# Performance work log

Measured on AMD Instinct MI355X. Metric: run time of the kernel, lower is better.

The kernel has to match this reference:

```python
import jax, jax.numpy as jnp
import numpy as np

B, S, D, H, HD, LY, DY = 2, 2048, 2048, 16, 128, 512, 2048
EPS_QK = 1e-5   # torch LayerNorm default for q_norm/k_norm
EPS_KY = 1e-6   # ky_norm eps


def _layernorm(x, w, b, eps):
    mu = jnp.mean(x, axis=-1, keepdims=True)
    var = jnp.mean(jnp.square(x - mu), axis=-1, keepdims=True)
    return (x - mu) * jax.lax.rsqrt(var + eps) * w + b


def _rope(t, freqs_cis):
    # t: [b, s, h, d]; freqs_cis: [s, d//2, 2] = (cos, sin)
    b, s, h, d = t.shape
    t2 = t.reshape(b, s, h, d // 2, 2)
    cos = freqs_cis[None, :, None, :, 0]
    sin = freqs_cis[None, :, None, :, 1]
    r0 = t2[..., 0] * cos - t2[..., 1] * sin
    r1 = t2[..., 0] * sin + t2[..., 1] * cos
    return jnp.stack([r0, r1], axis=-1).reshape(b, s, h, d)


def _attn(q, k, v, kv_mask, scale):
    # q: [b,s,h,d], k/v: [b,t,h,d], kv_mask: [b,t] bool
    scores = jnp.einsum('bshd,bthd->bhst', q, k) * scale
    neg = jnp.finfo(scores.dtype).min
    scores = jnp.where(kv_mask[:, None, None, :], scores, neg)
    p = jax.nn.softmax(scores, axis=-1)
    return jnp.einsum('bhst,bthd->bshd', p, v)


def setup_inputs() -> dict:
    key = jax.random.key(0)
    ks = jax.random.split(key, 20)
    x = jax.random.normal(ks[0], (B, S, D), jnp.float32)
    y = jax.random.normal(ks[1], (B, LY, DY), jnp.float32)
    x_mask = jnp.ones((B, S), jnp.bool_)
    y_mask = jnp.ones((B, LY), jnp.bool_)
    # RoPE table, theta=10000
    pos = jnp.arange(S, dtype=jnp.float32)
    inv = 1.0 / (10000.0 ** (jnp.arange(0, HD, 2, dtype=jnp.float32) / HD))
    ang = pos[:, None] * inv[None, :]                      # [S, HD//2]
    freqs_cis = jnp.stack([jnp.cos(ang), jnp.sin(ang)], -1)  # [S, HD//2, 2]
    sd = 0.02
    wq = sd * jax.random.normal(ks[2], (D, H * HD), jnp.float32)
    wk = sd * jax.random.normal(ks[3], (D, H * HD), jnp.float32)
    wv = sd * jax.random.normal(ks[4], (D, H * HD), jnp.float32)
    wo = sd * jax.random.normal(ks[5], (H * HD, D), jnp.float32)
    wky = sd * jax.random.normal(ks[6], (DY, H * HD), jnp.float32)
    wvy = sd * jax.random.normal(ks[7], (DY, H * HD), jnp.float32)
    gate = 0.1 * jax.random.normal(ks[8], (H,), jnp.float32)  # nn.Parameter (zeros init; randomized for nontrivial test)
    qn_w = 1.0 + 0.01 * jax.random.normal(ks[9], (H * HD,), jnp.float32)
    qn_b = 0.01 * jax.random.normal(ks[10], (H * HD,), jnp.float32)
    kn_w = 1.0 + 0.01 * jax.random.normal(ks[11], (H * HD,), jnp.float32)
    kn_b = 0.01 * jax.random.normal(ks[12], (H * HD,), jnp.float32)
    kyn_w = 1.0 + 0.01 * jax.random.normal(ks[13], (H * HD,), jnp.float32)
    kyn_b = 0.01 * jax.random.normal(ks[14], (H * HD,), jnp.float32)
    return dict(x=x, x_mask=x_mask, freqs_cis=freqs_cis, y=y, y_mask=y_mask,
                wq=wq, wk=wk, wv=wv, wo=wo, wky=wky, wvy=wvy, gate=gate,
                qn_w=qn_w, qn_b=qn_b, kn_w=kn_w, kn_b=kn_b, kyn_w=kyn_w, kyn_b=kyn_b)


def reference(x, x_mask, freqs_cis, y, y_mask, wq, wk, wv, wo, wky, wvy, gate,
              qn_w, qn_b, kn_w, kn_b, kyn_w, kyn_b):
    batch, seq_len, _ = x.shape
    xq = x @ wq
    xk = x @ wk
    xv = x @ wv
    # qk_norm with qk_bias=True: LayerNorm over full n_heads*head_dim channels
    xq = _layernorm(xq, qn_w, qn_b, EPS_QK)
    xk = _layernorm(xk, kn_w, kn_b, EPS_QK)
    xq = xq.reshape(batch, seq_len, H, HD)
    xk = xk.reshape(batch, seq_len, H, HD)
    xv = xv.reshape(batch, seq_len, H, HD)
    # n_kv_heads == n_heads: no repeat_interleave needed
    xq = _rope(xq, freqs_cis)
    xk = _rope(xk, freqs_cis)
    scale = 1.0 / jnp.sqrt(jnp.float32(HD))  # softmax_scale=None -> 1/sqrt(head_dim)
    output = _attn(xq, xk, xv, x_mask, scale)            # [b,s,h,d]
    # cross-attention branch (y_dim > 0); no RoPE on yk
    yk = _layernorm(y @ wky, kyn_w, kyn_b, EPS_KY).reshape(batch, -1, H, HD)
    yv = (y @ wvy).reshape(batch, -1, H, HD)
    output_y = _attn(xq, yk, yv, y_mask, scale)
    output_y = output_y * jnp.tanh(gate)[None, None, :, None]
    output = output + output_y
    out = output.reshape(batch, seq_len, H * HD) @ wo
    return out
```

## Files before the change

### kernel.cpp

```cpp
#include <hip/hip_runtime.h>

typedef unsigned short u16;
typedef __attribute__((ext_vector_type(8))) short short8;
typedef __attribute__((ext_vector_type(4))) unsigned short ushort4v;
typedef __attribute__((ext_vector_type(8))) unsigned short ushort8v;
typedef __attribute__((ext_vector_type(4))) float f32x4;

#define MFMA_16x16x32(a, b, c) __builtin_amdgcn_mfma_f32_16x16x32_bf16(a, b, c, 0, 0, 0)

#define GLOAD16(g, l)                                                              \
    __builtin_amdgcn_global_load_lds(                                              \
        (const __attribute__((address_space(1))) unsigned int*)(g),                \
        (__attribute__((address_space(3))) unsigned int*)(l), 16, 0, 0)

__device__ __forceinline__ u16 f2bf(float f) {
    unsigned int u = __float_as_uint(f);
    u += 0x7fffu + ((u >> 16) & 1u);
    return (u16)(u >> 16);
}

__global__ __launch_bounds__(256) void k_cast(const float* __restrict__ in, u16* __restrict__ out) {
    long i = ((long)blockIdx.x * 256 + threadIdx.x) * 8;
    f32x4 a = *(const f32x4*)(in + i);
    f32x4 b = *(const f32x4*)(in + i + 4);
    ushort8v o;
    o[0] = f2bf(a[0]); o[1] = f2bf(a[1]); o[2] = f2bf(a[2]); o[3] = f2bf(a[3]);
    o[4] = f2bf(b[0]); o[5] = f2bf(b[1]); o[6] = f2bf(b[2]); o[7] = f2bf(b[3]);
    *(ushort8v*)(out + i) = o;
}

__global__ __launch_bounds__(256) void k_tcast(const float* __restrict__ in, u16* __restrict__ out,
                                               int R, int C, long ibs, long obs) {
    __shared__ float tile[32][33];
    const int t = threadIdx.x;
    const int tx = t & 31, ty = t >> 5;
    const long r0 = (long)blockIdx.y * 32, c0 = (long)blockIdx.x * 32;
    const float* ip = in + (long)blockIdx.z * ibs;
    u16* op = out + (long)blockIdx.z * obs;
#pragma unroll
    for (int i = 0; i < 4; i++)
        tile[ty + 8 * i][tx] = ip[(r0 + ty + 8 * i) * C + c0 + tx];
    __syncthreads();
#pragma unroll
    for (int i = 0; i < 4; i++)
        op[(c0 + ty + 8 * i) * R + r0 + tx] = f2bf(tile[tx][ty + 8 * i]);
}

__device__ __forceinline__ void gemm_body(const u16* __restrict__ A, const u16* __restrict__ Bt,
                                          float* __restrict__ C, int N, int K) {
    __shared__ u16 As[128 * 32];
    __shared__ u16 Bs[128 * 32];
    const int t = threadIdx.x;
    const int lane = t & 63, wave = t >> 6;
    const long m0 = (long)blockIdx.y * 128, n0 = (long)blockIdx.x * 128;
    const int wm = (wave >> 1) * 64, wn = (wave & 1) * 64;
    const u16* Ag = A + (m0 + (t >> 2)) * (long)K + (t & 3) * 8;
    const u16* Bg = Bt + (n0 + (t >> 2)) * (long)K + (t & 3) * 8;
    u16* lA = As + wave * 512;
    u16* lB = Bs + wave * 512;
    const int fr = lane & 15, fg = (lane >> 4) * 8;
    const f32x4 z = {0.f, 0.f, 0.f, 0.f};
    f32x4 acc[4][4];
#pragma unroll
    for (int i = 0; i < 4; i++)
#pragma unroll
        for (int j = 0; j < 4; j++) acc[i][j] = z;
    for (int k0 = 0; k0 < K; k0 += 32) {
        __syncthreads();
        GLOAD16(Ag + k0, lA);
        GLOAD16(Ag + (long)64 * K + k0, lA + 2048);
        GLOAD16(Bg + k0, lB);
        GLOAD16(Bg + (long)64 * K + k0, lB + 2048);
        __syncthreads();
        short8 af[4], bf[4];
#pragma unroll
        for (int i = 0; i < 4; i++) {
            af[i] = *(const short8*)&As[(wm + i * 16 + fr) * 32 + fg];
            bf[i] = *(const short8*)&Bs[(wn + i * 16 + fr) * 32 + fg];
        }
#pragma unroll
        for (int i = 0; i < 4; i++)
#pragma unroll
            for (int j = 0; j < 4; j++)
                acc[i][j] = MFMA_16x16x32(af[i], bf[j], acc[i][j]);
    }
    const int cr = (lane >> 4) * 4, cc = lane & 15;
#pragma unroll
    for (int i = 0; i < 4; i++)
#pragma unroll
        for (int j = 0; j < 4; j++)
#pragma unroll
            for (int r = 0; r < 4; r++)
                C[(m0 + wm + i * 16 + cr + r) * N + (n0 + wn + j * 16 + cc)] = acc[i][j][r];
}

__global__ __launch_bounds__(256) void k_gemm(const u16* __restrict__ A, const u16* __restrict__ Bt,
                                              float* __restrict__ C, int N, int K) {
    gemm_body(A, Bt, C, N, K);
}

__global__ __launch_bounds__(256) void k_gemm2(const u16* __restrict__ A,
                                               const u16* __restrict__ Bt0, const u16* __restrict__ Bt1,
                                               float* __restrict__ C0, float* __restrict__ C1,
                                               int N, int K) {
    gemm_body(A, blockIdx.z ? Bt1 : Bt0, blockIdx.z ? C1 : C0, N, K);
}

__global__ __launch_bounds__(256) void k_ln(const float* __restrict__ in, const float* __restrict__ w,
                                            const float* __restrict__ bia, const float* __restrict__ freqs,
                                            u16* __restrict__ out, int Srows, float eps, int do_rope) {
    const int row = blockIdx.x;
    const int bi = row / Srows, s = row - bi * Srows;
    const int t = threadIdx.x;
    const long base = (long)row * 2048 + t * 8;
    f32x4 v0 = *(const f32x4*)(in + base);
    f32x4 v1 = *(const f32x4*)(in + base + 4);
    float sum = 0.f, sq = 0.f;
#pragma unroll
    for (int r = 0; r < 4; r++) {
        sum += v0[r] + v1[r];
        sq += v0[r] * v0[r] + v1[r] * v1[r];
    }
#pragma unroll
    for (int off = 32; off >= 1; off >>= 1) {
        sum += __shfl_xor(sum, off);
        sq += __shfl_xor(sq, off);
    }
    __shared__ float red[8];
    const int wv = t >> 6, lane = t & 63;
    if (lane == 0) { red[wv] = sum; red[4 + wv] = sq; }
    __syncthreads();
    sum = red[0] + red[1] + red[2] + red[3];
    sq  = red[4] + red[5] + red[6] + red[7];
    const float mu = sum * (1.f / 2048.f);
    const float rstd = rsqrtf(sq * (1.f / 2048.f) - mu * mu + eps);
    const int c0 = t * 8;
    f32x4 w0 = *(const f32x4*)(w + c0), w1 = *(const f32x4*)(w + c0 + 4);
    f32x4 b0 = *(const f32x4*)(bia + c0), b1 = *(const f32x4*)(bia + c0 + 4);
    float nv[8];
#pragma unroll
    for (int r = 0; r < 4; r++) {
        nv[r]     = (v0[r] - mu) * rstd * w0[r] + b0[r];
        nv[4 + r] = (v1[r] - mu) * rstd * w1[r] + b1[r];
    }
    if (do_rope) {
        const float* fp = freqs + ((long)s * 64 + ((c0 & 127) >> 1)) * 2;
        f32x4 f0 = *(const f32x4*)(fp), f1 = *(const f32x4*)(fp + 4);
        float t0, t1;
        t0 = nv[0]; t1 = nv[1]; nv[0] = t0 * f0[0] - t1 * f0[1]; nv[1] = t0 * f0[1] + t1 * f0[0];
        t0 = nv[2]; t1 = nv[3]; nv[2] = t0 * f0[2] - t1 * f0[3]; nv[3] = t0 * f0[3] + t1 * f0[2];
        t0 = nv[4]; t1 = nv[5]; nv[4] = t0 * f1[0] - t1 * f1[1]; nv[5] = t0 * f1[1] + t1 * f1[0];
        t0 = nv[6]; t1 = nv[7]; nv[6] = t0 * f1[2] - t1 * f1[3]; nv[7] = t0 * f1[3] + t1 * f1[2];
    }
    const int h = c0 >> 7;
    ushort8v o;
#pragma unroll
    for (int r = 0; r < 8; r++) o[r] = f2bf(nv[r]);
    *(ushort8v*)(out + (((long)bi * 16 + h) * Srows + s) * 128 + (c0 & 127)) = o;
}

__global__ __launch_bounds__(256, 4) void k_attn(const u16* __restrict__ Q, const u16* __restrict__ Kg,
                                                 const u16* __restrict__ Vt, const u16* __restrict__ Yk,
                                                 const u16* __restrict__ Yvt, const float* __restrict__ gate,
                                                 u16* __restrict__ Out) {
    __shared__ u16 Ks[2][32 * 128];
    __shared__ u16 Vs[2][128 * 32];
    __shared__ u16 Ps[4][16 * 40];
    const int t = threadIdx.x, lane = t & 63, wave = t >> 6;
    const int h = blockIdx.y, b = blockIdx.z;
    const int q0 = blockIdx.x * 64 + wave * 16;
    const long bh = (long)b * 16 + h;
    const int fr = lane & 15;
    const int g = lane >> 4;
    const int fg8 = g * 8;
    const float scale = 0.08838834764831845f;
    const f32x4 z = {0.f, 0.f, 0.f, 0.f};

    const int kr0 = (wave * 2 + 0) * 4 + (lane >> 4);
    const int kr1 = (wave * 2 + 1) * 4 + (lane >> 4);
    const int kc0 = ((lane & 15) ^ (kr0 & 7)) * 8;
    const int kc1 = ((lane & 15) ^ (kr1 & 7)) * 8;
    const int vr0 = (wave * 2 + 0) * 16 + (lane >> 2);
    const int vr1 = (wave * 2 + 1) * 16 + (lane >> 2);
    const int vc = (lane & 3) * 8;

    const u16* qp = Q + (bh * 2048 + q0 + fr) * 128;
    short8 qf[4];
#pragma unroll
    for (int ks = 0; ks < 4; ks++) qf[ks] = *(const short8*)(qp + fg8 + ks * 32);

    f32x4 o1[8], o2[8];
    const int sw = (fr & 7) * 8;

    auto stage = [&](int buf, const u16* kp, const u16* vp, int kb, long vstride) {
        GLOAD16(kp + (long)(kb + kr0) * 128 + kc0, &Ks[buf][(wave * 2 + 0) * 512]);
        GLOAD16(kp + (long)(kb + kr1) * 128 + kc1, &Ks[buf][(wave * 2 + 1) * 512]);
        GLOAD16(vp + (long)vr0 * vstride + kb + vc, &Vs[buf][(wave * 2 + 0) * 512]);
        GLOAD16(vp + (long)vr1 * vstride + kb + vc, &Vs[buf][(wave * 2 + 1) * 512]);
    };

    auto flash = [&](const u16* kp, const u16* vp, int L, long vstride, f32x4* oout) {
        float m = -3.0e38f, l = 0.f;
        f32x4 oacc[8];
#pragma unroll
        for (int i = 0; i < 8; i++) oacc[i] = z;
        stage(0, kp, vp, 0, vstride);
        __syncthreads();
        const int nt = L / 32;
        for (int ti = 0; ti < nt; ti++) {
            const int cur = ti & 1;
            if (ti + 1 < nt) stage(cur ^ 1, kp, vp, (ti + 1) * 32, vstride);
            f32x4 c0 = z, c1 = z;
#pragma unroll
            for (int ks = 0; ks < 4; ks++) {
                short8 k0f = *(const short8*)&Ks[cur][fr * 128 + ((fg8 + ks * 32) ^ sw)];
                short8 k1f = *(const short8*)&Ks[cur][(16 + fr) * 128 + ((fg8 + ks * 32) ^ sw)];
                c0 = MFMA_16x16x32(k0f, qf[ks], c0);
                c1 = MFMA_16x16x32(k1f, qf[ks], c1);
            }
            float s[8];
#pragma unroll
            for (int r = 0; r < 4; r++) { s[r] = c0[r] * scale; s[4 + r] = c1[r] * scale; }
            float tmax = s[0];
#pragma unroll
            for (int r = 1; r < 8; r++) tmax = fmaxf(tmax, s[r]);
            tmax = fmaxf(tmax, __shfl_xor(tmax, 16));
            tmax = fmaxf(tmax, __shfl_xor(tmax, 32));
            if (!__all(tmax <= m + 8.f)) {
                float mn = fmaxf(m, tmax);
                float corr = __expf(m - mn);
#pragma unroll
                for (int i = 0; i < 8; i++) oacc[i] *= corr;
                l *= corr;
                m = mn;
            }
            float p[8], ts = 0.f;
#pragma unroll
            for (int r = 0; r < 8; r++) { p[r] = __expf(s[r] - m); ts += p[r]; }
            ts += __shfl_xor(ts, 16);
            ts += __shfl_xor(ts, 32);
            l += ts;
            ushort4v pk0, pk1;
#pragma unroll
            for (int r = 0; r < 4; r++) { pk0[r] = f2bf(p[r]); pk1[r] = f2bf(p[4 + r]); }
            *(ushort4v*)&Ps[wave][fr * 40 + g * 4] = pk0;
            *(ushort4v*)&Ps[wave][fr * 40 + 16 + g * 4] = pk1;
            short8 pf = *(const short8*)&Ps[wave][fr * 40 + fg8];
#pragma unroll
            for (int dt = 0; dt < 8; dt++) {
                short8 vf = *(const short8*)&Vs[cur][(dt * 16 + fr) * 32 + fg8];
                oacc[dt] = MFMA_16x16x32(vf, pf, oacc[dt]);
            }
            __syncthreads();
        }
        float inv = 1.f / l;
#pragma unroll
        for (int i = 0; i < 8; i++) oout[i] = oacc[i] * inv;
    };

    flash(Kg + bh * 2048 * 128, Vt + bh * 128 * 2048, 2048, 2048, o1);
    flash(Yk + bh * 512 * 128, Yvt + bh * 128 * 512, 512, 512, o2);

    const float tg = tanhf(gate[h]);
    u16* op = Out + ((long)b * 2048 + q0 + fr) * 2048 + h * 128;
#pragma unroll
    for (int dt = 0; dt < 8; dt++) {
        ushort4v w4;
#pragma unroll
        for (int r = 0; r < 4; r++) w4[r] = f2bf(o1[dt][r] + tg * o2[dt][r]);
        *(ushort4v*)(op + dt * 16 + g * 4) = w4;
    }
}

extern "C" void kernel_launch(void* const* d_in, const int* in_sizes, int n_in,
                              void* d_out, int out_size, void* d_ws, size_t ws_size,
                              hipStream_t stream) {
    (void)in_sizes; (void)n_in; (void)out_size; (void)ws_size;
    const float* x     = (const float*)d_in[0];
    const float* freqs = (const float*)d_in[2];
    const float* y     = (const float*)d_in[3];
    const float* wq    = (const float*)d_in[5];
    const float* wk    = (const float*)d_in[6];
    const float* wv    = (const float*)d_in[7];
    const float* wo    = (const float*)d_in[8];
    const float* wky   = (const float*)d_in[9];
    const float* wvy   = (const float*)d_in[10];
    const float* gate  = (const float*)d_in[11];
    const float* qn_w  = (const float*)d_in[12];
    const float* qn_b  = (const float*)d_in[13];
    const float* kn_w  = (const float*)d_in[14];
    const float* kn_b  = (const float*)d_in[15];
    const float* kyn_w = (const float*)d_in[16];
    const float* kyn_b = (const float*)d_in[17];
    float* out = (float*)d_out;

    char* p = (char*)d_ws;
    u16* xb   = (u16*)p; p += 4096L * 2048 * 2;
    u16* yb   = (u16*)p; p += 1024L * 2048 * 2;
    u16* wT   = (u16*)p; p += 2048L * 2048 * 2;
    u16* qb   = (u16*)p; p += 4096L * 2048 * 2;
    u16* kbuf = (u16*)p; p += 4096L * 2048 * 2;
    u16* vtb  = (u16*)p; p += 4096L * 2048 * 2;
    u16* ykb  = (u16*)p; p += 1024L * 2048 * 2;
    u16* yvtb = (u16*)p; p += 1024L * 2048 * 2;
    u16* aob  = (u16*)p; p += 4096L * 2048 * 2;
    float* raw = out;
    u16* wT2   = ykb;
    float* rawB = (float*)aob;

    k_cast<<<dim3(4096), dim3(256), 0, stream>>>(x, xb);
    k_cast<<<dim3(1024), dim3(256), 0, stream>>>(y, yb);

    k_tcast<<<dim3(64, 64, 1), dim3(256), 0, stream>>>(wq, wT, 2048, 2048, 0, 0);
    k_gemm<<<dim3(16, 32), dim3(256), 0, stream>>>(xb, wT, raw, 2048, 2048);
    k_ln<<<dim3(4096), dim3(256), 0, stream>>>(raw, qn_w, qn_b, freqs, qb, 2048, 1e-5f, 1);
    k_tcast<<<dim3(64, 64, 1), dim3(256), 0, stream>>>(wk, wT, 2048, 2048, 0, 0);
    k_gemm<<<dim3(16, 32), dim3(256), 0, stream>>>(xb, wT, raw, 2048, 2048);
    k_ln<<<dim3(4096), dim3(256), 0, stream>>>(raw, kn_w, kn_b, freqs, kbuf, 2048, 1e-5f, 1);
    k_tcast<<<dim3(64, 64, 1), dim3(256), 0, stream>>>(wv, wT, 2048, 2048, 0, 0);
    k_gemm<<<dim3(16, 32), dim3(256), 0, stream>>>(xb, wT, raw, 2048, 2048);
    k_tcast<<<dim3(64, 64, 2), dim3(256), 0, stream>>>(raw, vtb, 2048, 2048, 2048L * 2048, 2048L * 2048);
    k_tcast<<<dim3(64, 64, 1), dim3(256), 0, stream>>>(wky, wT, 2048, 2048, 0, 0);
    k_tcast<<<dim3(64, 64, 1), dim3(256), 0, stream>>>(wvy, wT2, 2048, 2048, 0, 0);
    k_gemm2<<<dim3(16, 8, 2), dim3(256), 0, stream>>>(yb, wT, wT2, raw, rawB, 2048, 2048);
    k_ln<<<dim3(1024), dim3(256), 0, stream>>>(raw, kyn_w, kyn_b, freqs, ykb, 512, 1e-6f, 0);
    k_tcast<<<dim3(64, 16, 2), dim3(256), 0, stream>>>(rawB, yvtb, 512, 2048, 512L * 2048, 2048L * 512);
    k_attn<<<dim3(32, 16, 2), dim3(256), 0, stream>>>(qb, kbuf, vtb, ykb, yvtb, gate, aob);
    k_tcast<<<dim3(64, 64, 1), dim3(256), 0, stream>>>(wo, wT, 2048, 2048, 0, 0);
    k_gemm<<<dim3(16, 32), dim3(256), 0, stream>>>(aob, wT, out, 2048, 2048);
}
```

Measured before the change: 662.3 us.

## Fuse Q/K/V projections into one GEMM launch with bf16 K/V outputs

Replaces three sequential x@W GEMMs with a single launch covering a 48-wide column grid that selects the Q, K or V weight per segment. Q keeps an fp32 output for LayerNorm, while K and V are written as bf16 and handled by new bf16-input LayerNorm and transpose kernels, which halves their intermediate traffic. The attention softmax switches to exp2 with log2e folded into the scale. In exchange, K is now rounded to bf16 before LayerNorm, which adds some precision loss, and more workspace buffers are aliased.

```diff
diff --git a/kernel.cpp b/kernel.cpp
--- a/kernel.cpp
+++ b/kernel.cpp
@@ -17,6 +17,9 @@
     unsigned int u = __float_as_uint(f);
     u += 0x7fffu + ((u >> 16) & 1u);
     return (u16)(u >> 16);
+}
+__device__ __forceinline__ float bf2f(u16 v) {
+    return __uint_as_float(((unsigned int)v) << 16);
 }
 
 __global__ __launch_bounds__(256) void k_cast(const float* __restrict__ in, u16* __restrict__ out) {
@@ -44,6 +47,23 @@
 #pragma unroll
     for (int i = 0; i < 4; i++)
         op[(c0 + ty + 8 * i) * R + r0 + tx] = f2bf(tile[tx][ty + 8 * i]);
+}
+
+__global__ __launch_bounds__(256) void k_tcast_bf(const u16* __restrict__ in, u16* __restrict__ out,
+                                                  int R, int C, long ibs, long obs) {
+    __shared__ u16 tile[32][34];
+    const int t = threadIdx.x;
+    const int tx = t & 31, ty = t >> 5;
+    const long r0 = (long)blockIdx.y * 32, c0 = (long)blockIdx.x * 32;
+    const u16* ip = in + (long)blockIdx.z * ibs;
+    u16* op = out + (long)blockIdx.z * obs;
+#pragma unroll
+    for (int i = 0; i < 4; i++)
+        tile[ty + 8 * i][tx] = ip[(r0 + ty + 8 * i) * C + c0 + tx];
+    __syncthreads();
+#pragma unroll
+    for (int i = 0; i < 4; i++)
+        op[(c0 + ty + 8 * i) * R + r0 + tx] = tile[tx][ty + 8 * i];
 }
 
 __device__ __forceinline__ void gemm_body(const u16* __restrict__ A, const u16* __restrict__ Bt,
@@ -106,21 +126,79 @@
     gemm_body(A, blockIdx.z ? Bt1 : Bt0, blockIdx.z ? C1 : C0, N, K);
 }
 
-__global__ __launch_bounds__(256) void k_ln(const float* __restrict__ in, const float* __restrict__ w,
-                                            const float* __restrict__ bia, const float* __restrict__ freqs,
-                                            u16* __restrict__ out, int Srows, float eps, int do_rope) {
-    const int row = blockIdx.x;
-    const int bi = row / Srows, s = row - bi * Srows;
-    const int t = threadIdx.x;
-    const long base = (long)row * 2048 + t * 8;
-    f32x4 v0 = *(const f32x4*)(in + base);
-    f32x4 v1 = *(const f32x4*)(in + base + 4);
+__global__ __launch_bounds__(256) void k_gemm3(const u16* __restrict__ A,
+                                               const u16* __restrict__ Bq, const u16* __restrict__ Bk,
+                                               const u16* __restrict__ Bv,
+                                               float* __restrict__ Cq, u16* __restrict__ Ck,
+                                               u16* __restrict__ Cv, int K) {
+    __shared__ u16 As[128 * 32];
+    __shared__ u16 Bs[128 * 32];
+    const int t = threadIdx.x;
+    const int lane = t & 63, wave = t >> 6;
+    const long m0 = (long)blockIdx.y * 128;
+    const int n0 = blockIdx.x * 128;
+    const int seg = n0 >> 11;
+    const int ncol = n0 & 2047;
+    const u16* Bt = (seg == 0) ? Bq : ((seg == 1) ? Bk : Bv);
+    const int wm = (wave >> 1) * 64, wn = (wave & 1) * 64;
+    const u16* Ag = A + (m0 + (t >> 2)) * (long)K + (t & 3) * 8;
+    const u16* Bg = Bt + (ncol + (t >> 2)) * (long)K + (t & 3) * 8;
+    u16* lA = As + wave * 512;
+    u16* lB = Bs + wave * 512;
+    const int fr = lane & 15, fg = (lane >> 4) * 8;
+    const f32x4 z = {0.f, 0.f, 0.f, 0.f};
+    f32x4 acc[4][4];
+#pragma unroll
+    for (int i = 0; i < 4; i++)
+#pragma unroll
+        for (int j = 0; j < 4; j++) acc[i][j] = z;
+    for (int k0 = 0; k0 < K; k0 += 32) {
+        __syncthreads();
+        GLOAD16(Ag + k0, lA);
+        GLOAD16(Ag + (long)64 * K + k0, lA + 2048);
+        GLOAD16(Bg + k0, lB);
+        GLOAD16(Bg + (long)64 * K + k0, lB + 2048);
+        __syncthreads();
+        short8 af[4], bf[4];
+#pragma unroll
+        for (int i = 0; i < 4; i++) {
+            af[i] = *(const short8*)&As[(wm + i * 16 + fr) * 32 + fg];
+            bf[i] = *(const short8*)&Bs[(wn + i * 16 + fr) * 32 + fg];
+        }
+#pragma unroll
+        for (int i = 0; i < 4; i++)
+#pragma unroll
+            for (int j = 0; j < 4; j++)
+                acc[i][j] = MFMA_16x16x32(af[i], bf[j], acc[i][j]);
+    }
+    const int cr = (lane >> 4) * 4, cc = lane & 15;
+    if (seg == 0) {
+#pragma unroll
+        for (int i = 0; i < 4; i++)
+#pragma unroll
+            for (int j = 0; j < 4; j++)
+#pragma unroll
+                for (int r = 0; r < 4; r++)
+                    Cq[(m0 + wm + i * 16 + cr + r) * 2048 + (ncol + wn + j * 16 + cc)] = acc[i][j][r];
+    } else {
+        u16* Co = (seg == 1) ? Ck : Cv;
+#pragma unroll
+        for (int i = 0; i < 4; i++)
+#pragma unroll
+            for (int j = 0; j < 4; j++)
+#pragma unroll
+                for (int r = 0; r < 4; r++)
+                    Co[(m0 + wm + i * 16 + cr + r) * 2048 + (ncol + wn + j * 16 + cc)] = f2bf(acc[i][j][r]);
+    }
+}
+
+__device__ __forceinline__ void ln_core(float nv[8], const float* __restrict__ w,
+                                        const float* __restrict__ bia, const float* __restrict__ freqs,
+                                        u16* __restrict__ out, int bi, int s, int Srows,
+                                        float eps, int do_rope, int t) {
     float sum = 0.f, sq = 0.f;
 #pragma unroll
-    for (int r = 0; r < 4; r++) {
-        sum += v0[r] + v1[r];
-        sq += v0[r] * v0[r] + v1[r] * v1[r];
-    }
+    for (int r = 0; r < 8; r++) { sum += nv[r]; sq += nv[r] * nv[r]; }
 #pragma unroll
     for (int off = 32; off >= 1; off >>= 1) {
         sum += __shfl_xor(sum, off);
@@ -137,11 +215,10 @@
     const int c0 = t * 8;
     f32x4 w0 = *(const f32x4*)(w + c0), w1 = *(const f32x4*)(w + c0 + 4);
     f32x4 b0 = *(const f32x4*)(bia + c0), b1 = *(const f32x4*)(bia + c0 + 4);
-    float nv[8];
 #pragma unroll
     for (int r = 0; r < 4; r++) {
-        nv[r]     = (v0[r] - mu) * rstd * w0[r] + b0[r];
-        nv[4 + r] = (v1[r] - mu) * rstd * w1[r] + b1[r];
+        nv[r]     = (nv[r] - mu) * rstd * w0[r] + b0[r];
+        nv[4 + r] = (nv[4 + r] - mu) * rstd * w1[r] + b1[r];
     }
     if (do_rope) {
         const float* fp = freqs + ((long)s * 64 + ((c0 & 127) >> 1)) * 2;
@@ -157,6 +234,32 @@
 #pragma unroll
     for (int r = 0; r < 8; r++) o[r] = f2bf(nv[r]);
     *(ushort8v*)(out + (((long)bi * 16 + h) * Srows + s) * 128 + (c0 & 127)) = o;
+}
+
+__global__ __launch_bounds__(256) void k_ln(const float* __restrict__ in, const float* __restrict__ w,
+                                            const float* __restrict__ bia, const float* __restrict__ freqs,
+                                            u16* __restrict__ out, int Srows, float eps, int do_rope) {
+    const int row = blockIdx.x;
+    const int bi = row / Srows, s = row - bi * Srows;
+    const int t = threadIdx.x;
+    const long base = (long)row * 2048 + t * 8;
+    f32x4 v0 = *(const f32x4*)(in + base);
+    f32x4 v1 = *(const f32x4*)(in + base + 4);
+    float nv[8] = {v0[0], v0[1], v0[2], v0[3], v1[0], v1[1], v1[2], v1[3]};
+    ln_core(nv, w, bia, freqs, out, bi, s, Srows, eps, do_rope, t);
+}
+
+__global__ __launch_bounds__(256) void k_ln_bf(const u16* __restrict__ in, const float* __restrict__ w,
+                                               const float* __restrict__ bia, const float* __restrict__ freqs,
+                                               u16* __restrict__ out, int Srows, float eps, int do_rope) {
+    const int row = blockIdx.x;
+    const int bi = row / Srows, s = row - bi * Srows;
+    const int t = threadIdx.x;
+    ushort8v v = *(const ushort8v*)(in + (long)row * 2048 + t * 8);
+    float nv[8];
+#pragma unroll
+    for (int r = 0; r < 8; r++) nv[r] = bf2f(v[r]);
+    ln_core(nv, w, bia, freqs, out, bi, s, Srows, eps, do_rope, t);
 }
 
 __global__ __launch_bounds__(256, 4) void k_attn(const u16* __restrict__ Q, const u16* __restrict__ Kg,
@@ -173,7 +276,7 @@
     const int fr = lane & 15;
     const int g = lane >> 4;
     const int fg8 = g * 8;
-    const float scale = 0.08838834764831845f;
+    const float scale2 = 0.08838834764831845f * 1.4426950408889634f;
     const f32x4 z = {0.f, 0.f, 0.f, 0.f};
 
     const int kr0 = (wave * 2 + 0) * 4 + (lane >> 4);
@@ -220,15 +323,15 @@
             }
             float s[8];
 #pragma unroll
-            for (int r = 0; r < 4; r++) { s[r] = c0[r] * scale; s[4 + r] = c1[r] * scale; }
-            float tmax = s[0];
-#pragma unroll
-            for (int r = 1; r < 8; r++) tmax = fmaxf(tmax, s[r]);
+            for (int r = 0; r < 4; r++) { s[r] = c0[r] * scale2; s[4 + r] = c1[r] * scale2; }
+            float t0 = fmaxf(fmaxf(s[0], s[1]), fmaxf(s[2], s[3]));
+            float t1 = fmaxf(fmaxf(s[4], s[5]), fmaxf(s[6], s[7]));
+            float tmax = fmaxf(t0, t1);
             tmax = fmaxf(tmax, __shfl_xor(tmax, 16));
             tmax = fmaxf(tmax, __shfl_xor(tmax, 32));
             if (!__all(tmax <= m + 8.f)) {
                 float mn = fmaxf(m, tmax);
-                float corr = __expf(m - mn);
+                float corr = exp2f(m - mn);
 #pragma unroll
                 for (int i = 0; i < 8; i++) oacc[i] *= corr;
                 l *= corr;
@@ -236,7 +339,7 @@
             }
             float p[8], ts = 0.f;
 #pragma unroll
-            for (int r = 0; r < 8; r++) { p[r] = __expf(s[r] - m); ts += p[r]; }
+            for (int r = 0; r < 8; r++) { p[r] = exp2f(s[r] - m); ts += p[r]; }
             ts += __shfl_xor(ts, 16);
             ts += __shfl_xor(ts, 32);
             l += ts;
@@ -305,6 +408,10 @@
     u16* yvtb = (u16*)p; p += 1024L * 2048 * 2;
     u16* aob  = (u16*)p; p += 4096L * 2048 * 2;
     float* raw = out;
+    u16* wTk   = qb;
+    u16* wTv   = kbuf;
+    u16* krawb = vtb;
+    u16* vrawb = aob;
     u16* wT2   = ykb;
     float* rawB = (float*)aob;
 
@@ -312,20 +419,21 @@
     k_cast<<<dim3(1024), dim3(256), 0, stream>>>(y, yb);
 
     k_tcast<<<dim3(64, 64, 1), dim3(256), 0, stream>>>(wq, wT, 2048, 2048, 0, 0);
-    k_gemm<<<dim3(16, 32), dim3(256), 0, stream>>>(xb, wT, raw, 2048, 2048);
+    k_tcast<<<dim3(64, 64, 1), dim3(256), 0, stream>>>(wk, wTk, 2048, 2048, 0, 0);
+    k_tcast<<<dim3(64, 64, 1), dim3(256), 0, stream>>>(wv, wTv, 2048, 2048, 0, 0);
+    k_gemm3<<<dim3(48, 32), dim3(256), 0, stream>>>(xb, wT, wTk, wTv, raw, krawb, vrawb, 2048);
     k_ln<<<dim3(4096), dim3(256), 0, stream>>>(raw, qn_w, qn_b, freqs, qb, 2048, 1e-5f, 1);
-    k_tcast<<<dim3(64, 64, 1), dim3(256), 0, stream>>>(wk, wT, 2048, 2048, 0, 0);
-    k_gemm<<<dim3(16, 32), dim3(256), 0, stream>>>(xb, wT, raw, 2048, 2048);
-    k_ln<<<dim3(4096), dim3(256), 0, stream>>>(raw, kn_w, kn_b, freqs, kbuf, 2048, 1e-5f, 1);
-    k_tcast<<<dim3(64, 64, 1), dim3(256), 0, stream>>>(wv, wT, 2048, 2048, 0, 0);
-    k_gemm<<<dim3(16, 32), dim3(256), 0, stream>>>(xb, wT, raw, 2048, 2048);
-    k_tcast<<<dim3(64, 64, 2), dim3(256), 0, stream>>>(raw, vtb, 2048, 2048, 2048L * 2048, 2048L * 2048);
+    k_ln_bf<<<dim3(4096), dim3(256), 0, stream>>>(krawb, kn_w, kn_b, freqs, kbuf, 2048, 1e-5f, 1);
+    k_tcast_bf<<<dim3(64, 64, 2), dim3(256), 0, stream>>>(vrawb, vtb, 2048, 2048, 2048L * 2048, 2048L * 2048);
+
     k_tcast<<<dim3(64, 64, 1), dim3(256), 0, stream>>>(wky, wT, 2048, 2048, 0, 0);
     k_tcast<<<dim3(64, 64, 1), dim3(256), 0, stream>>>(wvy, wT2, 2048, 2048, 0, 0);
     k_gemm2<<<dim3(16, 8, 2), dim3(256), 0, stream>>>(yb, wT, wT2, raw, rawB, 2048, 2048);
     k_ln<<<dim3(1024), dim3(256), 0, stream>>>(raw, kyn_w, kyn_b, freqs, ykb, 512, 1e-6f, 0);
     k_tcast<<<dim3(64, 16, 2), dim3(256), 0, stream>>>(rawB, yvtb, 512, 2048, 512L * 2048, 2048L * 512);
+
     k_attn<<<dim3(32, 16, 2), dim3(256), 0, stream>>>(qb, kbuf, vtb, ykb, yvtb, gate, aob);
+
     k_tcast<<<dim3(64, 64, 1), dim3(256), 0, stream>>>(wo, wT, 2048, 2048, 0, 0);
     k_gemm<<<dim3(16, 32), dim3(256), 0, stream>>>(aob, wT, out, 2048, 2048);
 }
```

Measured after the change: 641.9 us. -3.1%, faster.
